# Performance work log

Hardware: AMD Instinct MI355X
Metric: run time of the kernel (lower is better)

Reference implementation:

```python
import jax, jax.numpy as jnp
import numpy as np

B, D, C, M = 16384, 512, 1000, 8


def setup_inputs() -> dict:
    key = jax.random.key(0)
    k1, k2, k3, k4 = jax.random.split(key, 4)
    x = jax.random.normal(k1, (B, D), dtype=jnp.float32)
    W = jax.random.normal(k2, (M, D, C), dtype=jnp.float32) * 0.02
    b = jax.random.normal(k3, (M, C), dtype=jnp.float32) * 0.02
    coefs = jax.random.uniform(k4, (M,), dtype=jnp.float32, minval=0.5, maxval=1.5)
    return {"x": x, "W": W, "b": b, "coefs": coefs}


def reference(x, W, b, coefs):
    # Per-model logits: [M, B, C]
    logits = jnp.einsum('bd,mdc->mbc', x, W) + b[:, None, :]
    pos = jnp.argmax(logits, axis=-1)  # [M, B] predicted class per model/sample
    rows = jnp.broadcast_to(jnp.arange(x.shape[0])[None, :], pos.shape)  # [M, B]
    # Weighted vote scatter-add: ans[j, pos[m, j]] += coefs[m]
    ans = jnp.zeros((x.shape[0], W.shape[2]), dtype=jnp.float32)
    ans = ans.at[rows, pos].add(jnp.broadcast_to(coefs[:, None], pos.shape))
    return ans / W.shape[0]
```

## Files before the change

kernel.cpp:

```cpp
#include <hip/hip_runtime.h>

#define B_N 16384
#define D_K 512
#define C_N 1000
#define CP 1024
#define M_N 8
#define GAP_EPS 1e-3f

typedef __attribute__((ext_vector_type(8))) _Float16 f16x8;
typedef __attribute__((ext_vector_type(4))) float f32x4;

typedef const __attribute__((address_space(1))) unsigned int* gptr_t;
typedef __attribute__((address_space(3))) unsigned int* lptr_t;

__device__ __forceinline__ void gload16(const void* g, void* l) {
    __builtin_amdgcn_global_load_lds((gptr_t)g, (lptr_t)l, 16, 0, 0);
}

#define BAR()        asm volatile("s_barrier" ::: "memory")
#define WAIT_LGKM0() asm volatile("s_waitcnt lgkmcnt(0)" ::: "memory")
#define WAIT_VM4()   asm volatile("s_waitcnt vmcnt(4)" ::: "memory")
#define WAIT_VM0()   asm volatile("s_waitcnt vmcnt(0)" ::: "memory")

__device__ __forceinline__ unsigned short h16(float f) {
    _Float16 h = (_Float16)f;
    return *(unsigned short*)&h;
}


__global__ __launch_bounds__(256) void ve_conv(const float* __restrict__ x,
        const float* __restrict__ W, unsigned short* __restrict__ xf,
        unsigned short* __restrict__ wt, unsigned int* __restrict__ cnts) {
    const int tid = threadIdx.x;
    if (blockIdx.x < 8192) {
        int i = blockIdx.x * 256 + tid;
        if (blockIdx.x == 0 && tid < M_N) cnts[tid] = 0u;
        float4 v = reinterpret_cast<const float4*>(x)[i];
        ushort4 h;
        h.x = h16(v.x); h.y = h16(v.y); h.z = h16(v.z); h.w = h16(v.w);
        reinterpret_cast<ushort4*>(xf)[i] = h;
    } else {
        __shared__ float t[64][65];
        const int b = blockIdx.x - 8192;
        const int c0 = (b & 15) * 64, k0 = ((b >> 4) & 7) * 64, m = b >> 7;
#pragma unroll
        for (int p = 0; p < 16; ++p) {
            int idx = p * 256 + tid;
            int kk = idx >> 6, cc = idx & 63;
            int c = c0 + cc;
            t[kk][cc] = (c < C_N) ? W[((size_t)m * D_K + k0 + kk) * C_N + c] : 0.f;
        }
        __syncthreads();
#pragma unroll
        for (int p = 0; p < 4; ++p) {
            int idx = p * 256 + tid;
            int cc = idx >> 4, kq = idx & 15;
            ushort4 h;
            h.x = h16(t[kq * 4 + 0][cc]); h.y = h16(t[kq * 4 + 1][cc]);
            h.z = h16(t[kq * 4 + 2][cc]); h.w = h16(t[kq * 4 + 3][cc]);
            size_t o = ((size_t)m * CP + c0 + cc) * D_K + k0 + kq * 4;
            *reinterpret_cast<ushort4*>(wt + o) = h;
        }
    }
}


__global__ __launch_bounds__(256, 3) void ve_gemm16d(
        const unsigned short* __restrict__ Xf, const unsigned short* __restrict__ WT,
        const float* __restrict__ bias, float4* __restrict__ part) {
    __shared__ unsigned short At[12288];
    __shared__ unsigned short Bt[12288];

    const int tid = threadIdx.x;
    const int l = tid & 63, w = tid >> 6;
    const int wr = w >> 1, wc = w & 1;
    const int l15 = l & 15, kg = l >> 4;
    const int bid = blockIdx.x;
    const int mb = bid & 7, ct = (bid >> 3) & 7, rt = bid >> 6;
    const int r0 = rt * 128, c0 = ct * 128;

    const int lhi = l >> 3, llo = l & 7;
    const int s3g = llo ^ lhi;
    const int srow16 = (lhi << 1) | (s3g >> 2);
    const int kgs = (s3g & 3) * 8;

    const unsigned short* xA0 = Xf + (size_t)(r0 +      w * 16 + srow16) * D_K + kgs;
    const unsigned short* xA1 = Xf + (size_t)(r0 + 64 + w * 16 + srow16) * D_K + kgs;
    const unsigned short* xB0 = WT + (size_t)(mb * CP + c0 +      w * 16 + srow16) * D_K + kgs;
    const unsigned short* xB1 = WT + (size_t)(mb * CP + c0 + 64 + w * 16 + srow16) * D_K + kgs;

    auto stage = [&](int t, int buf) {
        unsigned short* A = At + buf * 4096;
        unsigned short* B = Bt + buf * 4096;
        gload16(xA0 + t * 32, A + tid * 8);
        gload16(xA1 + t * 32, A + 2048 + tid * 8);
        gload16(xB0 + t * 32, B + tid * 8);
        gload16(xB1 + t * 32, B + 2048 + tid * 8);
    };

    auto ldsoff = [&](int row, int kc) {
        return (row >> 1) * 64 + (((((row & 1) << 2) | kc) ^ ((row >> 1) & 7)) * 8);
    };
    const char* aP[4]; const char* bP[4];
#pragma unroll
    for (int i = 0; i < 4; ++i) {
        aP[i] = (const char*)At + 2 * ldsoff(wr * 64 + i * 16 + l15, kg);
        bP[i] = (const char*)Bt + 2 * ldsoff(wc * 64 + i * 16 + l15, kg);
    }

    f32x4 acc[4][4];
#pragma unroll
    for (int i = 0; i < 4; ++i)
#pragma unroll
        for (int j = 0; j < 4; ++j) acc[i][j] = (f32x4){0.f, 0.f, 0.f, 0.f};

    stage(0, 0);
    stage(1, 1);
    WAIT_VM4();
    BAR();

#pragma unroll
    for (int t = 0; t < 16; ++t) {
        if (t < 14) stage(t + 2, (t + 2) % 3);
        const int cur = (t % 3) * 8192;

        f16x8 af[4], bf[4];
#pragma unroll
        for (int i = 0; i < 4; ++i) af[i] = *reinterpret_cast<const f16x8*>(aP[i] + cur);
#pragma unroll
        for (int j = 0; j < 4; ++j) bf[j] = *reinterpret_cast<const f16x8*>(bP[j] + cur);
#pragma unroll
        for (int i = 0; i < 4; ++i)
#pragma unroll
            for (int j = 0; j < 4; ++j)
                acc[i][j] = __builtin_amdgcn_mfma_f32_16x16x32_f16(af[i], bf[j], acc[i][j], 0, 0, 0);

        if (t < 14)       { WAIT_VM4(); }
        else if (t == 14) { WAIT_VM0(); }
        WAIT_LGKM0();
        BAR();
    }

    float4 (*wtop)[2] = reinterpret_cast<float4(*)[2]>(At);

    float bv[4]; int cg[4];
#pragma unroll
    for (int j = 0; j < 4; ++j) {
        int c = c0 + wc * 64 + j * 16 + l15;
        cg[j] = c;
        bv[j] = (c < C_N) ? bias[mb * C_N + c] : -1e30f;
    }
#pragma unroll
    for (int i = 0; i < 4; ++i) {
#pragma unroll
        for (int reg = 0; reg < 4; ++reg) {
            float v1 = acc[i][0][reg] + bv[0]; int i1 = cg[0];
            float v2 = -1e30f;
#pragma unroll
            for (int j = 1; j < 4; ++j) {
                float v = acc[i][j][reg] + bv[j];
                float mn = fminf(v, v1);
                v2 = fmaxf(v2, mn);
                i1 = (v > v1) ? cg[j] : i1;
                v1 = fmaxf(v1, v);
            }
#pragma unroll
            for (int mask = 1; mask < 16; mask <<= 1) {
                float ov1 = __shfl_xor(v1, mask);
                int   oi1 = __shfl_xor(i1, mask);
                float ov2 = __shfl_xor(v2, mask);
                float mn = fminf(v1, ov1);
                v2 = fmaxf(fmaxf(v2, ov2), mn);
                i1 = (ov1 > v1) ? oi1 : i1;
                v1 = fmaxf(v1, ov1);
            }
            if (l15 == 0) {
                int row = wr * 64 + i * 16 + (l >> 4) * 4 + reg;
                wtop[row][wc] = make_float4(v1, __int_as_float(i1), v2, 0.f);
            }
        }
    }
    __syncthreads();
    if (tid < 128) {
        float4 a = wtop[tid][0], b = wtop[tid][1];
        float v1, v2; int i1;
        if (b.x > a.x) {
            v1 = b.x; i1 = __float_as_int(b.y);
            v2 = fmaxf(a.x, b.z);
        } else {
            v1 = a.x; i1 = __float_as_int(a.y);
            v2 = fmaxf(b.x, a.z);
        }
        part[((size_t)mb * B_N + r0 + tid) * 8 + ct] =
            make_float4(v1, __int_as_float(i1), v2, 0.f);
    }
}


__global__ __launch_bounds__(256) void ve_flag8(const float4* __restrict__ part,
        unsigned int* __restrict__ wout, unsigned int* __restrict__ rlist,
        unsigned int* __restrict__ cnts) {
    int r = blockIdx.x * 256 + threadIdx.x;
#pragma unroll
    for (int m = 0; m < M_N; ++m) {
        float4 o = part[((size_t)m * B_N + r) * 8 + 0];
        float v1 = o.x; int i1 = __float_as_int(o.y); float v2 = o.z;
#pragma unroll
        for (int t = 1; t < 8; ++t) {
            float4 q = part[((size_t)m * B_N + r) * 8 + t];
            if (q.x > v1) {
                v2 = fmaxf(v1, fmaxf(q.z, v2));
                v1 = q.x; i1 = __float_as_int(q.y);
            } else {
                v2 = fmaxf(v2, q.x);
            }
        }
        wout[m * B_N + r] = (unsigned)i1;
        if (v1 - v2 <= GAP_EPS) {
            unsigned pos = atomicAdd(&cnts[m], 1u);
            rlist[m * B_N + pos] = (unsigned)r;
        }
    }
}


__global__ __launch_bounds__(256) void ve_exact_g(
        const float* __restrict__ x, const float* __restrict__ W,
        const float* __restrict__ bias, const unsigned int* __restrict__ rlist,
        const unsigned int* __restrict__ cnts, float2* __restrict__ part2) {
    __shared__ float xs[32][129];
    __shared__ float wsm[32][128];
    __shared__ int rg[128];
    const int ct = blockIdx.x, m = blockIdx.z;
    const int tid = threadIdx.x;
    const int tx = tid & 15, ty = tid >> 4;
    const int c0 = ct * 128;
    const unsigned nm = cnts[m];

    for (unsigned rb = blockIdx.y; rb * 128 < nm; rb += gridDim.y) {
        __syncthreads();
        if (tid < 128) {
            unsigned idx = rb * 128 + tid;
            rg[tid] = (idx < nm) ? (int)rlist[m * B_N + idx] : 0;
        }
        __syncthreads();

        float acc[8][8];
#pragma unroll
        for (int i = 0; i < 8; i++)
#pragma unroll
            for (int j = 0; j < 8; j++) acc[i][j] = 0.f;

        for (int kt = 0; kt < D_K; kt += 32) {
#pragma unroll
            for (int i = 0; i < 4; i++) {
                int li = tid + i * 256;
                int row = li >> 3, kq = li & 7;
                float4 v = *reinterpret_cast<const float4*>(
                        x + (size_t)rg[row] * D_K + kt + kq * 4);
                int kk = kq * 4;
                xs[kk + 0][row] = v.x; xs[kk + 1][row] = v.y;
                xs[kk + 2][row] = v.z; xs[kk + 3][row] = v.w;
            }
#pragma unroll
            for (int i = 0; i < 4; i++) {
                int li = tid + i * 256;
                int kk = li >> 5, cq = li & 31;
                int c = c0 + cq * 4;
                const float* p = W + ((size_t)(m * D_K + kt + kk)) * C_N + c;
                float4 v;
                if (c + 3 < C_N) v = *reinterpret_cast<const float4*>(p);
                else {
                    v.x = (c + 0 < C_N) ? p[0] : 0.f; v.y = (c + 1 < C_N) ? p[1] : 0.f;
                    v.z = (c + 2 < C_N) ? p[2] : 0.f; v.w = (c + 3 < C_N) ? p[3] : 0.f;
                }
                wsm[kk][cq * 4 + 0] = v.x; wsm[kk][cq * 4 + 1] = v.y;
                wsm[kk][cq * 4 + 2] = v.z; wsm[kk][cq * 4 + 3] = v.w;
            }
            __syncthreads();
            for (int kk = 0; kk < 32; kk++) {
                float a[8], bb[8];
#pragma unroll
                for (int i = 0; i < 8; i++) a[i] = xs[kk][ty + i * 16];
#pragma unroll
                for (int j = 0; j < 8; j++) bb[j] = wsm[kk][tx + j * 16];
#pragma unroll
                for (int i = 0; i < 8; i++)
#pragma unroll
                    for (int j = 0; j < 8; j++) acc[i][j] += a[i] * bb[j];
            }
            __syncthreads();
        }

        const float NEG_INF = -__builtin_huge_valf();
        float bv[8]; int cv[8];
#pragma unroll
        for (int j = 0; j < 8; j++) {
            int c = c0 + tx + j * 16;
            cv[j] = c;
            bv[j] = (c < C_N) ? bias[m * C_N + c] : 0.f;
        }
#pragma unroll
        for (int i = 0; i < 8; i++) {
            float best = NEG_INF; int bidx = 0x7fffffff;
#pragma unroll
            for (int j = 0; j < 8; j++) {
                int c = cv[j];
                float v = (c < C_N) ? (acc[i][j] + bv[j]) : NEG_INF;
                if (v > best || (v == best && c < bidx)) { best = v; bidx = c; }
            }
#pragma unroll
            for (int mask = 1; mask < 16; mask <<= 1) {
                float ov = __shfl_xor(best, mask);
                int oi = __shfl_xor(bidx, mask);
                if (ov > best || (ov == best && oi < bidx)) { best = ov; bidx = oi; }
            }
            unsigned slot = rb * 128 + ty + i * 16;
            if (tx == 0 && slot < nm)
                part2[((size_t)m * B_N + slot) * 8 + ct] = make_float2(best, __int_as_float(bidx));
        }
    }
}

__global__ __launch_bounds__(256) void ve_merge_x(const float2* __restrict__ part2,
        const unsigned int* __restrict__ rlist, const unsigned int* __restrict__ cnts,
        unsigned int* __restrict__ wout) {
    int gid = blockIdx.x * 256 + threadIdx.x;
    int m = gid >> 14, s = gid & (B_N - 1);
    if (s < (int)cnts[m]) {
        const float NEG_INF = -__builtin_huge_valf();
        float best = NEG_INF; int bidx = 0x7fffffff;
#pragma unroll
        for (int ctt = 0; ctt < 8; ctt++) {
            float2 p = part2[((size_t)m * B_N + s) * 8 + ctt];
            int oi = __float_as_int(p.y);
            if (p.x > best || (p.x == best && oi < bidx)) { best = p.x; bidx = oi; }
        }
        wout[m * B_N + rlist[m * B_N + s]] = (unsigned)bidx;
    }
}

__global__ __launch_bounds__(256) void ve_votef(const unsigned int* __restrict__ wout,
        const float* __restrict__ coefs, float* __restrict__ out) {
    const int tid = threadIdx.x;
    float4* po = reinterpret_cast<float4*>(out) + (size_t)blockIdx.x * 64000;
    const float4 z = make_float4(0.f, 0.f, 0.f, 0.f);
    for (int i = 0; i < 250; ++i) po[i * 256 + tid] = z;
    __syncthreads();
    int r = blockIdx.x * 256 + tid;
#pragma unroll
    for (int m = 0; m < M_N; ++m)
        out[(size_t)r * C_N + wout[m * B_N + r]] += coefs[m] * 0.125f;
}


#define TM 128
#define TN 128
#define TK 32
#define CT 8

__global__ __launch_bounds__(256) void ve_zero_out(float* __restrict__ out, int n4) {
    int i = blockIdx.x * blockDim.x + threadIdx.x;
    const float4 z = make_float4(0.f, 0.f, 0.f, 0.f);
    for (; i < n4; i += gridDim.x * blockDim.x)
        reinterpret_cast<float4*>(out)[i] = z;
}

__global__ __launch_bounds__(256) void ve_gemm_argmax_fb(
        const float* __restrict__ x, const float* __restrict__ W,
        const float* __restrict__ bias, float2* __restrict__ part) {
    __shared__ float xs[TK][TM + 1];
    __shared__ float ws[TK][TN];
    const int ct = blockIdx.x, rt = blockIdx.y, m = blockIdx.z;
    const int tid = threadIdx.x;
    const int tx = tid & 15, ty = tid >> 4;
    const int r0 = rt * TM, c0 = ct * TN;
    float acc[8][8];
#pragma unroll
    for (int i = 0; i < 8; i++)
#pragma unroll
        for (int j = 0; j < 8; j++) acc[i][j] = 0.f;
    const float* xbase = x + (size_t)r0 * D_K;
    for (int kt = 0; kt < D_K; kt += TK) {
#pragma unroll
        for (int i = 0; i < 4; i++) {
            int li = tid + i * 256;
            int row = li >> 3, kq = li & 7;
            float4 v = *reinterpret_cast<const float4*>(xbase + (size_t)row * D_K + kt + kq * 4);
            int kk = kq * 4;
            xs[kk + 0][row] = v.x; xs[kk + 1][row] = v.y;
            xs[kk + 2][row] = v.z; xs[kk + 3][row] = v.w;
        }
#pragma unroll
        for (int i = 0; i < 4; i++) {
            int li = tid + i * 256;
            int kk = li >> 5, cq = li & 31;
            int c = c0 + cq * 4;
            const float* p = W + ((size_t)(m * D_K + kt + kk)) * C_N + c;
            float4 v;
            if (c + 3 < C_N) v = *reinterpret_cast<const float4*>(p);
            else {
                v.x = (c + 0 < C_N) ? p[0] : 0.f; v.y = (c + 1 < C_N) ? p[1] : 0.f;
                v.z = (c + 2 < C_N) ? p[2] : 0.f; v.w = (c + 3 < C_N) ? p[3] : 0.f;
            }
            ws[kk][cq * 4 + 0] = v.x; ws[kk][cq * 4 + 1] = v.y;
            ws[kk][cq * 4 + 2] = v.z; ws[kk][cq * 4 + 3] = v.w;
        }
        __syncthreads();
        for (int kk = 0; kk < TK; kk++) {
            float a[8], bb[8];
#pragma unroll
            for (int i = 0; i < 8; i++) a[i] = xs[kk][ty + i * 16];
#pragma unroll
            for (int j = 0; j < 8; j++) bb[j] = ws[kk][tx + j * 16];
#pragma unroll
            for (int i = 0; i < 8; i++)
#pragma unroll
                for (int j = 0; j < 8; j++) acc[i][j] += a[i] * bb[j];
        }
        __syncthreads();
    }
    const float NEG_INF = -__builtin_huge_valf();
    float bv[8]; int cv[8];
#pragma unroll
    for (int j = 0; j < 8; j++) {
        int c = c0 + tx + j * 16;
        cv[j] = c;
        bv[j] = (c < C_N) ? bias[m * C_N + c] : 0.f;
    }
#pragma unroll
    for (int i = 0; i < 8; i++) {
        int r = r0 + ty + i * 16;
        float best = NEG_INF; int bidx = 0x7fffffff;
#pragma unroll
        for (int j = 0; j < 8; j++) {
            int c = cv[j];
            float v = (c < C_N) ? (acc[i][j] + bv[j]) : NEG_INF;
            if (v > best || (v == best && c < bidx)) { best = v; bidx = c; }
        }
#pragma unroll
        for (int mask = 1; mask < 16; mask <<= 1) {
            float ov = __shfl_xor(best, mask);
            int oi = __shfl_xor(bidx, mask);
            if (ov > best || (ov == best && oi < bidx)) { best = ov; bidx = oi; }
        }
        if (tx == 0) part[((size_t)m * B_N + r) * CT + ct] = make_float2(best, __int_as_float(bidx));
    }
}

__global__ __launch_bounds__(256) void ve_vote_fb(const float2* __restrict__ part,
        const float* __restrict__ coefs, float* __restrict__ out) {
    int r = blockIdx.x * blockDim.x + threadIdx.x;
    if (r >= B_N) return;
    const float NEG_INF = -__builtin_huge_valf();
#pragma unroll
    for (int m = 0; m < M_N; m++) {
        float best = NEG_INF; int bidx = 0x7fffffff;
#pragma unroll
        for (int ctt = 0; ctt < CT; ctt++) {
            float2 p = part[((size_t)m * B_N + r) * CT + ctt];
            int oi = __float_as_int(p.y);
            if (p.x > best || (p.x == best && oi < bidx)) { best = p.x; bidx = oi; }
        }
        out[(size_t)r * C_N + bidx] += coefs[m] * 0.125f;
    }
}


extern "C" void kernel_launch(void* const* d_in, const int* in_sizes, int n_in,
                              void* d_out, int out_size, void* d_ws, size_t ws_size,
                              hipStream_t stream) {
    const float* x     = (const float*)d_in[0];
    const float* W     = (const float*)d_in[1];
    const float* bias  = (const float*)d_in[2];
    const float* coefs = (const float*)d_in[3];
    float* out = (float*)d_out;

    const size_t NEED = (57ull << 20) + 4096;
    if (ws_size >= NEED) {
        char* ws = (char*)d_ws;
        unsigned short* Xf    = (unsigned short*)(ws);
        unsigned short* WT16  = (unsigned short*)(ws + (16ull << 20));
        float4*         part  = (float4*)(ws + (24ull << 20));
        float2*         part2 = (float2*)(ws + (40ull << 20));
        unsigned int*   wout  = (unsigned int*)(ws + (48ull << 20));
        unsigned int*   rlist = (unsigned int*)(ws + (48ull << 20) + (512ull << 10));
        unsigned int*   cnts  = (unsigned int*)(ws + (49ull << 20));

        ve_conv<<<9216, 256, 0, stream>>>(x, W, Xf, WT16, cnts);
        ve_gemm16d<<<8192, 256, 0, stream>>>(Xf, WT16, bias, part);
        ve_flag8<<<64, 256, 0, stream>>>(part, wout, rlist, cnts);
        ve_exact_g<<<dim3(8, 4, 8), 256, 0, stream>>>(x, W, bias, rlist, cnts, part2);
        ve_merge_x<<<512, 256, 0, stream>>>(part2, rlist, cnts, wout);
        ve_votef<<<64, 256, 0, stream>>>(wout, coefs, out);
    } else {
        float2* partf = (float2*)d_ws;
        ve_zero_out<<<2048, 256, 0, stream>>>(out, B_N * C_N / 4);
        dim3 grid(CT, B_N / TM, M_N);
        ve_gemm_argmax_fb<<<grid, 256, 0, stream>>>(x, W, bias, partf);
        ve_vote_fb<<<(B_N + 255) / 256, 256, 0, stream>>>(partf, coefs, out);
    }
}
```

Baseline: 373.9 us.

## Widen GEMM column tile to 256 and merge four partial argmax slots

```diff
diff --git a/kernel.cpp b/kernel.cpp
--- a/kernel.cpp
+++ b/kernel.cpp
@@ -19,7 +19,7 @@
 
 #define BAR()        asm volatile("s_barrier" ::: "memory")
 #define WAIT_LGKM0() asm volatile("s_waitcnt lgkmcnt(0)" ::: "memory")
-#define WAIT_VM4()   asm volatile("s_waitcnt vmcnt(4)" ::: "memory")
+#define WAIT_VM6()   asm volatile("s_waitcnt vmcnt(6)" ::: "memory")
 #define WAIT_VM0()   asm volatile("s_waitcnt vmcnt(0)" ::: "memory")
 
 __device__ __forceinline__ unsigned short h16(float f) {
@@ -65,19 +65,19 @@
 }
 
 
-__global__ __launch_bounds__(256, 3) void ve_gemm16d(
+__global__ __launch_bounds__(256, 2) void ve_gemm16d(
         const unsigned short* __restrict__ Xf, const unsigned short* __restrict__ WT,
         const float* __restrict__ bias, float4* __restrict__ part) {
     __shared__ unsigned short At[12288];
-    __shared__ unsigned short Bt[12288];
+    __shared__ unsigned short Bt[24576];
 
     const int tid = threadIdx.x;
     const int l = tid & 63, w = tid >> 6;
     const int wr = w >> 1, wc = w & 1;
     const int l15 = l & 15, kg = l >> 4;
     const int bid = blockIdx.x;
-    const int mb = bid & 7, ct = (bid >> 3) & 7, rt = bid >> 6;
-    const int r0 = rt * 128, c0 = ct * 128;
+    const int mb = bid & 7, ct = (bid >> 3) & 3, rt = bid >> 5;
+    const int r0 = rt * 128, c0 = ct * 256;
 
     const int lhi = l >> 3, llo = l & 7;
     const int s3g = llo ^ lhi;
@@ -86,56 +86,66 @@
 
     const unsigned short* xA0 = Xf + (size_t)(r0 +      w * 16 + srow16) * D_K + kgs;
     const unsigned short* xA1 = Xf + (size_t)(r0 + 64 + w * 16 + srow16) * D_K + kgs;
-    const unsigned short* xB0 = WT + (size_t)(mb * CP + c0 +      w * 16 + srow16) * D_K + kgs;
-    const unsigned short* xB1 = WT + (size_t)(mb * CP + c0 + 64 + w * 16 + srow16) * D_K + kgs;
+    const unsigned short* xB0 = WT + (size_t)(mb * CP + c0 +       w * 16 + srow16) * D_K + kgs;
+    const unsigned short* xB1 = WT + (size_t)(mb * CP + c0 +  64 + w * 16 + srow16) * D_K + kgs;
+    const unsigned short* xB2 = WT + (size_t)(mb * CP + c0 + 128 + w * 16 + srow16) * D_K + kgs;
+    const unsigned short* xB3 = WT + (size_t)(mb * CP + c0 + 192 + w * 16 + srow16) * D_K + kgs;
 
     auto stage = [&](int t, int buf) {
         unsigned short* A = At + buf * 4096;
-        unsigned short* B = Bt + buf * 4096;
+        unsigned short* B = Bt + buf * 8192;
         gload16(xA0 + t * 32, A + tid * 8);
         gload16(xA1 + t * 32, A + 2048 + tid * 8);
         gload16(xB0 + t * 32, B + tid * 8);
         gload16(xB1 + t * 32, B + 2048 + tid * 8);
+        gload16(xB2 + t * 32, B + 4096 + tid * 8);
+        gload16(xB3 + t * 32, B + 6144 + tid * 8);
     };
 
     auto ldsoff = [&](int row, int kc) {
         return (row >> 1) * 64 + (((((row & 1) << 2) | kc) ^ ((row >> 1) & 7)) * 8);
     };
-    const char* aP[4]; const char* bP[4];
-#pragma unroll
-    for (int i = 0; i < 4; ++i) {
+    const char* aP[4]; const char* bP[8];
+#pragma unroll
+    for (int i = 0; i < 4; ++i)
         aP[i] = (const char*)At + 2 * ldsoff(wr * 64 + i * 16 + l15, kg);
-        bP[i] = (const char*)Bt + 2 * ldsoff(wc * 64 + i * 16 + l15, kg);
-    }
-
-    f32x4 acc[4][4];
+#pragma unroll
+    for (int j = 0; j < 8; ++j)
+        bP[j] = (const char*)Bt + wc * 8192 + (j >> 2) * 8192
+              + 2 * ldsoff((j & 3) * 16 + ((j >> 2) ? 0 : 0) + l15, kg);
+#pragma unroll
+    for (int j = 0; j < 8; ++j)
+        bP[j] = (const char*)Bt + wc * 8192 + 2 * ldsoff(j * 16 + l15, kg);
+
+    f32x4 acc[4][8];
 #pragma unroll
     for (int i = 0; i < 4; ++i)
 #pragma unroll
-        for (int j = 0; j < 4; ++j) acc[i][j] = (f32x4){0.f, 0.f, 0.f, 0.f};
+        for (int j = 0; j < 8; ++j) acc[i][j] = (f32x4){0.f, 0.f, 0.f, 0.f};
 
     stage(0, 0);
     stage(1, 1);
-    WAIT_VM4();
+    WAIT_VM6();
     BAR();
 
-#pragma unroll
+#pragma unroll 1
     for (int t = 0; t < 16; ++t) {
         if (t < 14) stage(t + 2, (t + 2) % 3);
-        const int cur = (t % 3) * 8192;
-
-        f16x8 af[4], bf[4];
-#pragma unroll
-        for (int i = 0; i < 4; ++i) af[i] = *reinterpret_cast<const f16x8*>(aP[i] + cur);
-#pragma unroll
-        for (int j = 0; j < 4; ++j) bf[j] = *reinterpret_cast<const f16x8*>(bP[j] + cur);
+        const int curA = (t % 3) * 8192;
+        const int curB = (t % 3) * 16384;
+
+        f16x8 af[4], bf[8];
+#pragma unroll
+        for (int i = 0; i < 4; ++i) af[i] = *reinterpret_cast<const f16x8*>(aP[i] + curA);
+#pragma unroll
+        for (int j = 0; j < 8; ++j) bf[j] = *reinterpret_cast<const f16x8*>(bP[j] + curB);
 #pragma unroll
         for (int i = 0; i < 4; ++i)
 #pragma unroll
-            for (int j = 0; j < 4; ++j)
+            for (int j = 0; j < 8; ++j)
                 acc[i][j] = __builtin_amdgcn_mfma_f32_16x16x32_f16(af[i], bf[j], acc[i][j], 0, 0, 0);
 
-        if (t < 14)       { WAIT_VM4(); }
+        if (t < 14)       { WAIT_VM6(); }
         else if (t == 14) { WAIT_VM0(); }
         WAIT_LGKM0();
         BAR();
@@ -143,10 +153,10 @@
 
     float4 (*wtop)[2] = reinterpret_cast<float4(*)[2]>(At);
 
-    float bv[4]; int cg[4];
-#pragma unroll
-    for (int j = 0; j < 4; ++j) {
-        int c = c0 + wc * 64 + j * 16 + l15;
+    float bv[8]; int cg[8];
+#pragma unroll
+    for (int j = 0; j < 8; ++j) {
+        int c = c0 + wc * 128 + j * 16 + l15;
         cg[j] = c;
         bv[j] = (c < C_N) ? bias[mb * C_N + c] : -1e30f;
     }
@@ -157,7 +167,7 @@
             float v1 = acc[i][0][reg] + bv[0]; int i1 = cg[0];
             float v2 = -1e30f;
 #pragma unroll
-            for (int j = 1; j < 4; ++j) {
+            for (int j = 1; j < 8; ++j) {
                 float v = acc[i][j][reg] + bv[j];
                 float mn = fminf(v, v1);
                 v2 = fmaxf(v2, mn);
@@ -191,23 +201,23 @@
             v1 = a.x; i1 = __float_as_int(a.y);
             v2 = fmaxf(b.x, a.z);
         }
-        part[((size_t)mb * B_N + r0 + tid) * 8 + ct] =
+        part[((size_t)mb * B_N + r0 + tid) * 4 + ct] =
             make_float4(v1, __int_as_float(i1), v2, 0.f);
     }
 }
 
 
-__global__ __launch_bounds__(256) void ve_flag8(const float4* __restrict__ part,
+__global__ __launch_bounds__(256) void ve_flag4(const float4* __restrict__ part,
         unsigned int* __restrict__ wout, unsigned int* __restrict__ rlist,
         unsigned int* __restrict__ cnts) {
     int r = blockIdx.x * 256 + threadIdx.x;
 #pragma unroll
     for (int m = 0; m < M_N; ++m) {
-        float4 o = part[((size_t)m * B_N + r) * 8 + 0];
+        float4 o = part[((size_t)m * B_N + r) * 4 + 0];
         float v1 = o.x; int i1 = __float_as_int(o.y); float v2 = o.z;
 #pragma unroll
-        for (int t = 1; t < 8; ++t) {
-            float4 q = part[((size_t)m * B_N + r) * 8 + t];
+        for (int t = 1; t < 4; ++t) {
+            float4 q = part[((size_t)m * B_N + r) * 4 + t];
             if (q.x > v1) {
                 v2 = fmaxf(v1, fmaxf(q.z, v2));
                 v1 = q.x; i1 = __float_as_int(q.y);
@@ -488,8 +498,8 @@
         unsigned int*   cnts  = (unsigned int*)(ws + (49ull << 20));
 
         ve_conv<<<9216, 256, 0, stream>>>(x, W, Xf, WT16, cnts);
-        ve_gemm16d<<<8192, 256, 0, stream>>>(Xf, WT16, bias, part);
-        ve_flag8<<<64, 256, 0, stream>>>(part, wout, rlist, cnts);
+        ve_gemm16d<<<4096, 256, 0, stream>>>(Xf, WT16, bias, part);
+        ve_flag4<<<64, 256, 0, stream>>>(part, wout, rlist, cnts);
         ve_exact_g<<<dim3(8, 4, 8), 256, 0, stream>>>(x, W, bias, rlist, cnts, part2);
         ve_merge_x<<<512, 256, 0, stream>>>(part2, rlist, cnts, wout);
         ve_votef<<<64, 256, 0, stream>>>(wout, coefs, out);
```

New measurement: 348.8 us. -6.7%, faster.
